# Performance work log

Measured on AMD Instinct MI355X. Metric: run time of the kernel, lower is better.

The kernel has to match this reference:

```python
import jax, jax.numpy as jnp
import numpy as np

E = 8192   # line-graph nodes (edges of g)
N = 4096   # graph nodes
FIN = 64   # in_feats
FOUT = 64  # out_feats
H = FOUT // 2
BN_EPS = 1e-5


def _linear_params(k, fan_in):
    kw, kb = jax.random.split(k)
    s = 1.0 / np.sqrt(fan_in)
    w = jax.random.uniform(kw, (H, fan_in), jnp.float32, -s, s)
    b = jax.random.uniform(kb, (H,), jnp.float32, -s, s)
    return w, b


def setup_inputs() -> dict:
    key = jax.random.key(0)
    ks = jax.random.split(key, 12)
    inp = {}
    inp["y"] = jax.random.normal(ks[0], (E, FIN), jnp.float32)
    inp["deg_g"] = jax.random.uniform(ks[1], (N,), jnp.float32)  # unused in forward
    inp["g_a1"] = jnp.zeros((N, N), jnp.float32)                  # unused in forward
    # adjacency-like 0/1 matrices, sparse pattern stored dense (as th.mm expects)
    inp["lg_a1"] = (jax.random.uniform(ks[2], (E, E)) < (8.0 / E)).astype(jnp.float32)
    inp["pm"] = (jax.random.uniform(ks[3], (N, E)) < (2.0 / N)).astype(jnp.float32)
    inp["pd"] = (jax.random.uniform(ks[4], (N, E)) < (2.0 / N)).astype(jnp.float32)
    inp["theta_y_w"], inp["theta_y_b"] = _linear_params(ks[5], FIN)
    inp["theta_y_r_w"], inp["theta_y_r_b"] = _linear_params(ks[6], FIN)
    inp["gamma_a_w"], inp["gamma_a_b"] = _linear_params(ks[7], FIN)
    inp["gamma_x_w"], inp["gamma_x_b"] = _linear_params(ks[8], FOUT)
    inp["gamma_a_r_w"], inp["gamma_a_r_b"] = _linear_params(ks[9], FIN)
    inp["gamma_x_r_w"], inp["gamma_x_r_b"] = _linear_params(ks[10], FOUT)
    inp["bn_x_w"] = jnp.ones((FOUT,), jnp.float32)
    inp["bn_x_b"] = jnp.zeros((FOUT,), jnp.float32)
    inp["bn_y_w"] = jnp.ones((FOUT,), jnp.float32)
    inp["bn_y_b"] = jnp.zeros((FOUT,), jnp.float32)
    return inp


def _bn(x, w, b):
    # BatchNorm2d on [B, C, 1, 1] in training mode == per-channel batch norm
    # with biased variance over the row (batch) dimension.
    m = x.mean(0)
    v = jnp.mean((x - m) ** 2, axis=0)
    return (x - m) * jax.lax.rsqrt(v + BN_EPS) * w + b


def reference(y, deg_g, g_a1, lg_a1, pm, pd,
              theta_y_w, theta_y_b, theta_y_r_w, theta_y_r_b,
              gamma_a_w, gamma_a_b, gamma_x_w, gamma_x_b,
              gamma_a_r_w, gamma_a_r_b, gamma_x_r_w, gamma_x_r_b,
              bn_x_w, bn_x_b, bn_y_w, bn_y_b):
    pd_y = pd @ y                                        # [N, FIN]
    x_r = pd_y @ theta_y_r_w.T + theta_y_r_b             # [N, H]
    x = pd_y @ theta_y_w.T + theta_y_b                   # [N, H]
    x = jnp.concatenate([x, jax.nn.relu(x_r)], axis=1)   # [N, FOUT]
    x = _bn(x, bn_x_w, bn_x_b)
    pm_x = pm.T @ x                                      # [E, FOUT]
    lg_y = lg_a1 @ y                                     # [E, FIN] (computed once; torch computes it twice, same math)
    y_r = (lg_y @ gamma_a_r_w.T + gamma_a_r_b) + (pm_x @ gamma_x_r_w.T + gamma_x_r_b)
    y_n = (lg_y @ gamma_a_w.T + gamma_a_b) + (pm_x @ gamma_x_w.T + gamma_x_b)
    y_out = jnp.concatenate([y_n, jax.nn.relu(y_r)], axis=1)  # [E, FOUT]
    return _bn(y_out, bn_y_w, bn_y_b)
```

## Files before the change

kernel.cpp:

```cpp
#include <hip/hip_runtime.h>

typedef unsigned int uint_t;
typedef unsigned short ushort_t;
typedef unsigned long long ull_t;

#define SLOTS 48

__device__ __forceinline__ float bcast(float v, int k) {
    union { float f; int i; } x; x.f = v;
    int r = __builtin_amdgcn_readlane(x.i, k);
    union { int i; float f; } y2; y2.i = r;
    return y2.f;
}

__global__ __launch_bounds__(256) void stream_kernel(
    const float* __restrict__ lg, const float* __restrict__ pd,
    const float* __restrict__ pm,
    ushort_t* __restrict__ keys, uint_t* __restrict__ counts)
{
    const int lane = threadIdx.x & 63;
    const int wid = blockIdx.x * 4 + (threadIdx.x >> 6);
    const float* A;
    int row;
    if (wid < 8192)       { row = wid;         A = lg; }
    else if (wid < 12288) { row = wid - 8192;  A = pd; }
    else                  { row = wid - 12288; A = pm; }

    const uint4* ap = (const uint4*)(A + (size_t)row * 8192);
    ushort_t* slice = keys + (size_t)wid * SLOTS;
    const ull_t lt = (1ull << lane) - 1ull;

    uint4 buf[8];
    #pragma unroll
    for (int i = 0; i < 8; ++i) buf[i] = ap[i * 64 + lane];

    uint_t cnt = 0;
    #pragma unroll
    for (int pp = 0; pp < 32; pp += 8) {
        #pragma unroll
        for (int i = 0; i < 8; ++i) {
            uint4 c = buf[i];
            if (pp + 8 + i < 32) buf[i] = ap[(pp + 8 + i) * 64 + lane];
            uint_t a0 = c.x, a1 = c.y, a2 = c.z, a3 = c.w;
            ull_t m = __ballot((a0 | a1 | a2 | a3) != 0u);
            if (m) {
                ull_t m0 = __ballot(a0 != 0u);
                ull_t m1 = __ballot(a1 != 0u);
                ull_t m2 = __ballot(a2 != 0u);
                ull_t m3 = __ballot(a3 != 0u);
                uint_t c0 = (uint_t)__popcll(m0), c1 = (uint_t)__popcll(m1);
                uint_t c2 = (uint_t)__popcll(m2);
                uint_t o0 = cnt + (uint_t)__popcll(m0 & lt);
                uint_t o1 = cnt + c0 + (uint_t)__popcll(m1 & lt);
                uint_t o2 = cnt + c0 + c1 + (uint_t)__popcll(m2 & lt);
                uint_t o3 = cnt + c0 + c1 + c2 + (uint_t)__popcll(m3 & lt);
                int j = (pp + i) * 256 + lane * 4;
                if (a0 && o0 < SLOTS) slice[o0] = (ushort_t)(j + 0);
                if (a1 && o1 < SLOTS) slice[o1] = (ushort_t)(j + 1);
                if (a2 && o2 < SLOTS) slice[o2] = (ushort_t)(j + 2);
                if (a3 && o3 < SLOTS) slice[o3] = (ushort_t)(j + 3);
                cnt += (uint_t)(__popcll(m0) + __popcll(m1) +
                                __popcll(m2) + __popcll(m3));
            }
        }
    }
    if (lane == 0) counts[wid] = (cnt > SLOTS) ? SLOTS : cnt;
}

__global__ __launch_bounds__(256) void gather_kernel(
    const ushort_t* __restrict__ keys, const uint_t* __restrict__ counts,
    const float* __restrict__ y,
    float* __restrict__ lg_y, float* __restrict__ pd_y)
{
    const int lane = threadIdx.x & 63;
    const int wid = blockIdx.x * 4 + (threadIdx.x >> 6);
    const ushort_t* slice = keys + (size_t)wid * SLOTS;
    uint_t cnt = counts[wid];
    float a0 = 0.f, a1 = 0.f, a2 = 0.f, a3 = 0.f;
    uint_t i = 0;
    for (; i + 4 <= cnt; i += 4) {
        int j0 = slice[i + 0], j1 = slice[i + 1];
        int j2 = slice[i + 2], j3 = slice[i + 3];
        a0 += y[(size_t)j0 * 64 + lane];
        a1 += y[(size_t)j1 * 64 + lane];
        a2 += y[(size_t)j2 * 64 + lane];
        a3 += y[(size_t)j3 * 64 + lane];
    }
    for (; i < cnt; ++i) a0 += y[(size_t)slice[i] * 64 + lane];
    float acc = (a0 + a1) + (a2 + a3);
    if (wid < 8192) lg_y[(size_t)wid * 64 + lane] = acc;
    else            pd_y[(size_t)(wid - 8192) * 64 + lane] = acc;
}

__global__ __launch_bounds__(256) void xlin_kernel(
    const float* __restrict__ pd_y,
    const float* __restrict__ wt, const float* __restrict__ bt,
    const float* __restrict__ wr, const float* __restrict__ br,
    float* __restrict__ x_raw, float* __restrict__ stats_x)
{
    __shared__ float red[2][4][64];
    const int wave = threadIdx.x >> 6, lane = threadIdx.x & 63;
    const float* wsrc = (lane < 32) ? (wt + lane * 64) : (wr + (lane - 32) * 64);
    float wreg[64];
    const float4* wp = (const float4*)wsrc;
    #pragma unroll
    for (int q = 0; q < 16; ++q) {
        float4 t = wp[q];
        wreg[q * 4 + 0] = t.x; wreg[q * 4 + 1] = t.y;
        wreg[q * 4 + 2] = t.z; wreg[q * 4 + 3] = t.w;
    }
    float bias = (lane < 32) ? bt[lane] : br[lane - 32];
    float s1 = 0.f, s2 = 0.f;
    const int row0 = (blockIdx.x * 4 + wave) * 8;
    for (int r = 0; r < 8; ++r) {
        int row = row0 + r;
        float xv = pd_y[(size_t)row * 64 + lane];
        float acc = bias;
        #pragma unroll
        for (int k = 0; k < 64; ++k) acc = fmaf(bcast(xv, k), wreg[k], acc);
        if (lane >= 32) acc = fmaxf(acc, 0.f);
        x_raw[(size_t)row * 64 + lane] = acc;
        s1 += acc; s2 += acc * acc;
    }
    red[0][wave][lane] = s1; red[1][wave][lane] = s2;
    __syncthreads();
    if (wave == 0) {
        float a = 0.f, b = 0.f;
        #pragma unroll
        for (int w = 0; w < 4; ++w) { a += red[0][w][lane]; b += red[1][w][lane]; }
        atomicAdd(&stats_x[lane], a);
        atomicAdd(&stats_x[64 + lane], b);
    }
}

__global__ __launch_bounds__(256) void scatter_kernel(
    const ushort_t* __restrict__ keys, const uint_t* __restrict__ counts,
    const float* __restrict__ x_raw, const float* __restrict__ stats_x,
    const float* __restrict__ bnxw, const float* __restrict__ bnxb,
    float* __restrict__ pm_x)
{
    const int lane = threadIdx.x & 63;
    const int row = blockIdx.x * 4 + (threadIdx.x >> 6);
    float mean = stats_x[lane] * (1.f / 4096.f);
    float var  = fmaxf(stats_x[64 + lane] * (1.f / 4096.f) - mean * mean, 0.f);
    float rstd = rsqrtf(var + 1e-5f);
    float scale = rstd * bnxw[lane];
    float shift = bnxb[lane] - mean * scale;
    const int wid = 12288 + row;
    const ushort_t* slice = keys + (size_t)wid * SLOTS;
    uint_t cnt = counts[wid];
    float xb = fmaf(x_raw[(size_t)row * 64 + lane], scale, shift);
    for (uint_t i = 0; i < cnt; ++i) {
        int e = slice[i];
        atomicAdd(&pm_x[(size_t)e * 64 + lane], xb);
    }
}

__global__ __launch_bounds__(256) void ylin_kernel(
    const float* __restrict__ lg_y, const float* __restrict__ pm_x,
    const float* __restrict__ wa, const float* __restrict__ ba,
    const float* __restrict__ wx, const float* __restrict__ bx,
    const float* __restrict__ war, const float* __restrict__ bar,
    const float* __restrict__ wxr, const float* __restrict__ bxr,
    float* __restrict__ yraw, float* __restrict__ stats_y)
{
    __shared__ float red[2][4][64];
    const int wave = threadIdx.x >> 6, lane = threadIdx.x & 63;
    const float* s1p = (lane < 32) ? (wa + lane * 64) : (war + (lane - 32) * 64);
    const float* s2p = (lane < 32) ? (wx + lane * 64) : (wxr + (lane - 32) * 64);
    float w1[64], w2[64];
    {
        const float4* p1 = (const float4*)s1p;
        const float4* p2 = (const float4*)s2p;
        #pragma unroll
        for (int q = 0; q < 16; ++q) {
            float4 t1 = p1[q], t2 = p2[q];
            w1[q * 4 + 0] = t1.x; w1[q * 4 + 1] = t1.y;
            w1[q * 4 + 2] = t1.z; w1[q * 4 + 3] = t1.w;
            w2[q * 4 + 0] = t2.x; w2[q * 4 + 1] = t2.y;
            w2[q * 4 + 2] = t2.z; w2[q * 4 + 3] = t2.w;
        }
    }
    float bias = (lane < 32) ? (ba[lane] + bx[lane])
                             : (bar[lane - 32] + bxr[lane - 32]);
    float s1 = 0.f, s2 = 0.f;
    const int row0 = (blockIdx.x * 4 + wave) * 8;
    for (int r = 0; r < 8; ++r) {
        int row = row0 + r;
        float lv = lg_y[(size_t)row * 64 + lane];
        float pv = pm_x[(size_t)row * 64 + lane];
        float acc = bias;
        #pragma unroll
        for (int k = 0; k < 64; ++k) {
            acc = fmaf(bcast(lv, k), w1[k], acc);
            acc = fmaf(bcast(pv, k), w2[k], acc);
        }
        if (lane >= 32) acc = fmaxf(acc, 0.f);
        yraw[(size_t)row * 64 + lane] = acc;
        s1 += acc; s2 += acc * acc;
    }
    red[0][wave][lane] = s1; red[1][wave][lane] = s2;
    __syncthreads();
    if (wave == 0) {
        float a = 0.f, b = 0.f;
        #pragma unroll
        for (int w = 0; w < 4; ++w) { a += red[0][w][lane]; b += red[1][w][lane]; }
        atomicAdd(&stats_y[lane], a);
        atomicAdd(&stats_y[64 + lane], b);
    }
}

__global__ __launch_bounds__(256) void bny_kernel(
    float* __restrict__ yraw, const float* __restrict__ stats_y,
    const float* __restrict__ bnyw, const float* __restrict__ bnyb)
{
    int idx = blockIdx.x * 256 + threadIdx.x;
    int c = idx & 63;
    float mean = stats_y[c] * (1.f / 8192.f);
    float var  = fmaxf(stats_y[64 + c] * (1.f / 8192.f) - mean * mean, 0.f);
    float rstd = rsqrtf(var + 1e-5f);
    yraw[idx] = (yraw[idx] - mean) * rstd * bnyw[c] + bnyb[c];
}

extern "C" void kernel_launch(void* const* d_in, const int* in_sizes, int n_in,
                              void* d_out, int out_size, void* d_ws, size_t ws_size,
                              hipStream_t stream)
{
    const float* y     = (const float*)d_in[0];
    const float* lg_a1 = (const float*)d_in[3];
    const float* pm    = (const float*)d_in[4];
    const float* pd    = (const float*)d_in[5];
    const float* th_w  = (const float*)d_in[6];
    const float* th_b  = (const float*)d_in[7];
    const float* thr_w = (const float*)d_in[8];
    const float* thr_b = (const float*)d_in[9];
    const float* ga_w  = (const float*)d_in[10];
    const float* ga_b  = (const float*)d_in[11];
    const float* gx_w  = (const float*)d_in[12];
    const float* gx_b  = (const float*)d_in[13];
    const float* gar_w = (const float*)d_in[14];
    const float* gar_b = (const float*)d_in[15];
    const float* gxr_w = (const float*)d_in[16];
    const float* gxr_b = (const float*)d_in[17];
    const float* bnx_w = (const float*)d_in[18];
    const float* bnx_b = (const float*)d_in[19];
    const float* bny_w = (const float*)d_in[20];
    const float* bny_b = (const float*)d_in[21];

    char* ws = (char*)d_ws;
    float* stats_x = (float*)ws;
    float* stats_y = (float*)(ws + 1024);
    float* pm_x    = (float*)(ws + 2048);
    const size_t zero_bytes = 2048 + (size_t)8192 * 64 * 4;
    float* pd_y  = (float*)(ws + zero_bytes);
    float* lg_y  = pd_y + (size_t)4096 * 64;
    float* x_raw = lg_y + (size_t)8192 * 64;
    ushort_t* keys = (ushort_t*)(x_raw + (size_t)4096 * 64);
    uint_t* counts = (uint_t*)(keys + (size_t)16384 * SLOTS);
    float* yraw  = (float*)d_out;

    hipMemsetAsync(d_ws, 0, zero_bytes, stream);

    stream_kernel<<<4096, 256, 0, stream>>>(lg_a1, pd, pm, keys, counts);
    gather_kernel<<<3072, 256, 0, stream>>>(keys, counts, y, lg_y, pd_y);
    xlin_kernel<<<128, 256, 0, stream>>>(pd_y, th_w, th_b, thr_w, thr_b,
                                         x_raw, stats_x);
    scatter_kernel<<<1024, 256, 0, stream>>>(keys, counts, x_raw, stats_x,
                                             bnx_w, bnx_b, pm_x);
    ylin_kernel<<<256, 256, 0, stream>>>(lg_y, pm_x, ga_w, ga_b, gx_w, gx_b,
                                         gar_w, gar_b, gxr_w, gxr_b,
                                         yraw, stats_y);
    bny_kernel<<<2048, 256, 0, stream>>>(yraw, stats_y, bny_w, bny_b);
}
```

Baseline: 612.3 us.

## Interleave dense-matrix chunk streaming across waves with atomic slot allocation

The dense-to-sparse pass no longer gives each wave one full row. Each wave now streams 1KB chunks strided across the whole concatenated matrix set, with half as many blocks, and uses non-temporal loads. Because a row's chunks are spread across waves, slot offsets come from a per-row atomic counter that is zeroed by the existing memset. SLOTS rises to 64 and readers clamp the count. The aim is better DRAM streaming and load balance, at the cost of atomics and key order that is no longer deterministic.

Result: no change. 620.2 us (+1.3%).

```diff
diff --git a/kernel.cpp b/kernel.cpp
--- a/kernel.cpp
+++ b/kernel.cpp
@@ -3,8 +3,10 @@
 typedef unsigned int uint_t;
 typedef unsigned short ushort_t;
 typedef unsigned long long ull_t;
-
-#define SLOTS 48
+typedef uint_t nvec4 __attribute__((ext_vector_type(4)));
+
+#define SLOTS 64
+#define NWAVES 8192
 
 __device__ __forceinline__ float bcast(float v, int k) {
     union { float f; int i; } x; x.f = v;
@@ -20,51 +22,60 @@
 {
     const int lane = threadIdx.x & 63;
     const int wid = blockIdx.x * 4 + (threadIdx.x >> 6);
-    const float* A;
-    int row;
-    if (wid < 8192)       { row = wid;         A = lg; }
-    else if (wid < 12288) { row = wid - 8192;  A = pd; }
-    else                  { row = wid - 12288; A = pm; }
-
-    const uint4* ap = (const uint4*)(A + (size_t)row * 8192);
-    ushort_t* slice = keys + (size_t)wid * SLOTS;
     const ull_t lt = (1ull << lane) - 1ull;
 
-    uint4 buf[8];
+    nvec4 buf[8];
     #pragma unroll
-    for (int i = 0; i < 8; ++i) buf[i] = ap[i * 64 + lane];
-
-    uint_t cnt = 0;
-    #pragma unroll
-    for (int pp = 0; pp < 32; pp += 8) {
-        #pragma unroll
-        for (int i = 0; i < 8; ++i) {
-            uint4 c = buf[i];
-            if (pp + 8 + i < 32) buf[i] = ap[(pp + 8 + i) * 64 + lane];
-            uint_t a0 = c.x, a1 = c.y, a2 = c.z, a3 = c.w;
-            ull_t m = __ballot((a0 | a1 | a2 | a3) != 0u);
-            if (m) {
-                ull_t m0 = __ballot(a0 != 0u);
-                ull_t m1 = __ballot(a1 != 0u);
-                ull_t m2 = __ballot(a2 != 0u);
-                ull_t m3 = __ballot(a3 != 0u);
-                uint_t c0 = (uint_t)__popcll(m0), c1 = (uint_t)__popcll(m1);
-                uint_t c2 = (uint_t)__popcll(m2);
-                uint_t o0 = cnt + (uint_t)__popcll(m0 & lt);
-                uint_t o1 = cnt + c0 + (uint_t)__popcll(m1 & lt);
-                uint_t o2 = cnt + c0 + c1 + (uint_t)__popcll(m2 & lt);
-                uint_t o3 = cnt + c0 + c1 + c2 + (uint_t)__popcll(m3 & lt);
-                int j = (pp + i) * 256 + lane * 4;
-                if (a0 && o0 < SLOTS) slice[o0] = (ushort_t)(j + 0);
-                if (a1 && o1 < SLOTS) slice[o1] = (ushort_t)(j + 1);
-                if (a2 && o2 < SLOTS) slice[o2] = (ushort_t)(j + 2);
-                if (a3 && o3 < SLOTS) slice[o3] = (ushort_t)(j + 3);
-                cnt += (uint_t)(__popcll(m0) + __popcll(m1) +
-                                __popcll(m2) + __popcll(m3));
-            }
-        }
-    }
-    if (lane == 0) counts[wid] = (cnt > SLOTS) ? SLOTS : cnt;
+    for (int i = 0; i < 8; ++i) {
+        const int c = wid + NWAVES * i;
+        const int row = c >> 5;
+        const float* base; int rl;
+        if (row < 8192)       { base = lg; rl = row; }
+        else if (row < 12288) { base = pd; rl = row - 8192; }
+        else                  { base = pm; rl = row - 12288; }
+        const nvec4* p = (const nvec4*)(base + (size_t)rl * 8192 + (c & 31) * 256);
+        buf[i] = __builtin_nontemporal_load(p + lane);
+    }
+
+    for (int it = 0; it < 64; ++it) {
+        nvec4 cur = buf[it & 7];
+        const int c = wid + NWAVES * it;
+        if (it + 8 < 64) {
+            const int nc = wid + NWAVES * (it + 8);
+            const int nrow = nc >> 5;
+            const float* base; int rl;
+            if (nrow < 8192)       { base = lg; rl = nrow; }
+            else if (nrow < 12288) { base = pd; rl = nrow - 8192; }
+            else                   { base = pm; rl = nrow - 12288; }
+            const nvec4* p = (const nvec4*)(base + (size_t)rl * 8192 + (nc & 31) * 256);
+            buf[it & 7] = __builtin_nontemporal_load(p + lane);
+        }
+        uint_t a0 = cur.x, a1 = cur.y, a2 = cur.z, a3 = cur.w;
+        ull_t m = __ballot((a0 | a1 | a2 | a3) != 0u);
+        if (m) {
+            const int row = c >> 5;
+            ull_t m0 = __ballot(a0 != 0u);
+            ull_t m1 = __ballot(a1 != 0u);
+            ull_t m2 = __ballot(a2 != 0u);
+            ull_t m3 = __ballot(a3 != 0u);
+            uint_t c0 = (uint_t)__popcll(m0), c1 = (uint_t)__popcll(m1);
+            uint_t c2 = (uint_t)__popcll(m2), c3 = (uint_t)__popcll(m3);
+            uint_t total = c0 + c1 + c2 + c3;
+            uint_t base = 0;
+            if (lane == 0) base = atomicAdd(&counts[row], total);
+            base = (uint_t)__shfl((int)base, 0);
+            uint_t o0 = base + (uint_t)__popcll(m0 & lt);
+            uint_t o1 = base + c0 + (uint_t)__popcll(m1 & lt);
+            uint_t o2 = base + c0 + c1 + (uint_t)__popcll(m2 & lt);
+            uint_t o3 = base + c0 + c1 + c2 + (uint_t)__popcll(m3 & lt);
+            const int jb = (c & 31) * 256 + lane * 4;
+            ushort_t* sl = keys + (size_t)row * SLOTS;
+            if (a0 && o0 < SLOTS) sl[o0] = (ushort_t)(jb + 0);
+            if (a1 && o1 < SLOTS) sl[o1] = (ushort_t)(jb + 1);
+            if (a2 && o2 < SLOTS) sl[o2] = (ushort_t)(jb + 2);
+            if (a3 && o3 < SLOTS) sl[o3] = (ushort_t)(jb + 3);
+        }
+    }
 }
 
 __global__ __launch_bounds__(256) void gather_kernel(
@@ -75,7 +86,7 @@
     const int lane = threadIdx.x & 63;
     const int wid = blockIdx.x * 4 + (threadIdx.x >> 6);
     const ushort_t* slice = keys + (size_t)wid * SLOTS;
-    uint_t cnt = counts[wid];
+    uint_t cnt = counts[wid]; if (cnt > SLOTS) cnt = SLOTS;
     float a0 = 0.f, a1 = 0.f, a2 = 0.f, a3 = 0.f;
     uint_t i = 0;
     for (; i + 4 <= cnt; i += 4) {
@@ -148,7 +159,7 @@
     float shift = bnxb[lane] - mean * scale;
     const int wid = 12288 + row;
     const ushort_t* slice = keys + (size_t)wid * SLOTS;
-    uint_t cnt = counts[wid];
+    uint_t cnt = counts[wid]; if (cnt > SLOTS) cnt = SLOTS;
     float xb = fmaf(x_raw[(size_t)row * 64 + lane], scale, shift);
     for (uint_t i = 0; i < cnt; ++i) {
         int e = slice[i];
@@ -251,17 +262,17 @@
     float* stats_x = (float*)ws;
     float* stats_y = (float*)(ws + 1024);
     float* pm_x    = (float*)(ws + 2048);
-    const size_t zero_bytes = 2048 + (size_t)8192 * 64 * 4;
+    uint_t* counts = (uint_t*)(ws + 2048 + (size_t)8192 * 64 * 4);
+    const size_t zero_bytes = 2048 + (size_t)8192 * 64 * 4 + 16384 * 4;
     float* pd_y  = (float*)(ws + zero_bytes);
     float* lg_y  = pd_y + (size_t)4096 * 64;
     float* x_raw = lg_y + (size_t)8192 * 64;
     ushort_t* keys = (ushort_t*)(x_raw + (size_t)4096 * 64);
-    uint_t* counts = (uint_t*)(keys + (size_t)16384 * SLOTS);
     float* yraw  = (float*)d_out;
 
-    hipMemsetAsync(d_ws, 0, zero_bytes, stream);
-
-    stream_kernel<<<4096, 256, 0, stream>>>(lg_a1, pd, pm, keys, counts);
+    (void)hipMemsetAsync(d_ws, 0, zero_bytes, stream);
+
+    stream_kernel<<<2048, 256, 0, stream>>>(lg_a1, pd, pm, keys, counts);
     gather_kernel<<<3072, 256, 0, stream>>>(keys, counts, y, lg_y, pd_y);
     xlin_kernel<<<128, 256, 0, stream>>>(pd_y, th_w, th_b, thr_w, thr_b,
                                          x_raw, stats_x);
```
